# Optimization experiments

Hardware: AMD Instinct MI355X
Metric: run time of the kernel (lower is better)

The kernel has to match this reference:

```python
import jax, jax.numpy as jnp
import numpy as np

B, N, E, H = 4, 2048, 512, 8
D = E // H  # head dim = 64


def setup_inputs() -> dict:
    key = jax.random.key(0)
    ks = jax.random.split(key, 5)
    s = 1.0 / np.sqrt(E)
    return {
        "x": jax.random.normal(ks[0], (B, N, E), dtype=jnp.float32),
        "Wk": jax.random.normal(ks[1], (E, E), dtype=jnp.float32) * s,
        "bk": jax.random.normal(ks[2], (E,), dtype=jnp.float32) * s,
        "Wv": jax.random.normal(ks[3], (E, E), dtype=jnp.float32) * s,
        "bv": jax.random.normal(ks[4], (E,), dtype=jnp.float32) * s,
    }


def reference(x, Wk, bk, Wv, bv):
    b, n, e = x.shape
    # Linear projections (torch Linear: y = x @ W.T + b), split into heads.
    keys = (x @ Wk.T + bk).reshape(b, n, H, D).transpose(0, 2, 1, 3)    # b h n d
    values = (x @ Wv.T + bv).reshape(b, n, H, D).transpose(0, 2, 1, 3)  # b h n d
    # Q = K self-attention: scores [b, h, n, n]
    dotprod = jnp.einsum('bhnd,bhmd->bhnm', keys, keys)
    # softmax over last axis, then unusual POST-softmax scaling by sqrt(emb)
    att = jax.nn.softmax(dotprod, axis=-1) / jnp.sqrt(jnp.asarray(e, x.dtype))
    # dropout p=0 -> identity
    out = jnp.einsum('bhnm,bhmd->bhnd', att, values)
    return out.transpose(0, 2, 1, 3).reshape(b, n, e)
```

## Files before the change

### kernel.cpp

```cpp
#include <hip/hip_runtime.h>

typedef __bf16 bf16_t;
typedef bf16_t bf16x8 __attribute__((ext_vector_type(8)));
typedef float f32x4 __attribute__((ext_vector_type(4)));

#define NSEQ 2048
#define EMB 512
#define HEADS 8
#define HD 64
#define BATCH 4
#define LOG2E 1.4426950408889634f

#define MFMA16(a, b, c) __builtin_amdgcn_mfma_f32_16x16x32_bf16(a, b, c, 0, 0, 0)

__global__ __launch_bounds__(256, 2) void proj_kernel(
    const float* __restrict__ x,
    const float* __restrict__ Wk, const float* __restrict__ bk,
    const float* __restrict__ Wv, const float* __restrict__ bv,
    bf16_t* __restrict__ Kh, bf16_t* __restrict__ Vt)
{
  __shared__ union {
    struct {
      __align__(16) bf16_t A[2][128][40];
      __align__(16) bf16_t B[2][128][40];
    } s;
    __align__(16) bf16_t T[128][136];
  } u;

  const int t    = threadIdx.x;
  const int w    = t >> 6;
  const int lane = t & 63;
  const int quad = lane >> 4;
  const int l15  = lane & 15;
  const int wr   = w >> 1, wc = w & 1;
  const int m0   = blockIdx.x * 128;
  const int n0   = blockIdx.y * 128;
  const int zz   = (blockIdx.y >= 4);
  const float* __restrict__ W = zz ? Wv : Wk;
  const int nW = n0 - zz * 512;

  const int sr = t >> 3;
  const int sj = t & 7;
  const int sb = sj >> 2, sc = (sj & 3) * 8;

  float4 pa[4][2], pb[4][2];
  auto prefetch = [&](int k0) {
#pragma unroll
    for (int i = 0; i < 4; ++i) {
      const float* xa = x + (size_t)(m0 + sr + i * 32) * EMB + k0 + sj * 8;
      const float* wa = W + (size_t)(nW + sr + i * 32) * EMB + k0 + sj * 8;
      pa[i][0] = *(const float4*)xa; pa[i][1] = *(const float4*)(xa + 4);
      pb[i][0] = *(const float4*)wa; pb[i][1] = *(const float4*)(wa + 4);
    }
  };
  auto pack8 = [](float4 a, float4 b) -> bf16x8 {
    bf16x8 v;
    v[0] = (bf16_t)a.x; v[1] = (bf16_t)a.y; v[2] = (bf16_t)a.z; v[3] = (bf16_t)a.w;
    v[4] = (bf16_t)b.x; v[5] = (bf16_t)b.y; v[6] = (bf16_t)b.z; v[7] = (bf16_t)b.w;
    return v;
  };

  f32x4 acc[4][4] = {};
  prefetch(0);

  for (int it = 0; it < 8; ++it) {
    __syncthreads();
#pragma unroll
    for (int i = 0; i < 4; ++i) {
      *(bf16x8*)(&u.s.A[sb][sr + i * 32][sc]) = pack8(pa[i][0], pa[i][1]);
      *(bf16x8*)(&u.s.B[sb][sr + i * 32][sc]) = pack8(pb[i][0], pb[i][1]);
    }
    __syncthreads();
    if (it < 7) prefetch((it + 1) * 64);

    bf16x8 af[4][2], bf[4][2];
#pragma unroll
    for (int mt = 0; mt < 4; ++mt)
#pragma unroll
      for (int kk = 0; kk < 2; ++kk)
        af[mt][kk] = *(const bf16x8*)(&u.s.A[kk][wr * 64 + mt * 16 + l15][quad * 8]);
#pragma unroll
    for (int nt = 0; nt < 4; ++nt)
#pragma unroll
      for (int kk = 0; kk < 2; ++kk)
        bf[nt][kk] = *(const bf16x8*)(&u.s.B[kk][wc * 64 + nt * 16 + l15][quad * 8]);
#pragma unroll
    for (int kk = 0; kk < 2; ++kk)
#pragma unroll
      for (int mt = 0; mt < 4; ++mt)
#pragma unroll
        for (int nt = 0; nt < 4; ++nt)
          acc[mt][nt] = MFMA16(af[mt][kk], bf[nt][kk], acc[mt][nt]);
  }

  __syncthreads();

#pragma unroll
  for (int mt = 0; mt < 4; ++mt) {
#pragma unroll
    for (int nt = 0; nt < 4; ++nt) {
      const int F = wc * 64 + nt * 16 + l15;
      const int c = n0 + F;
      const float bb = zz ? bv[c - 512] : bk[c];
#pragma unroll
      for (int reg = 0; reg < 4; ++reg) {
        const int R = wr * 64 + mt * 16 + quad * 4 + reg;
        const float v = acc[mt][nt][reg] + bb;
        if (!zz) u.T[R][F] = (bf16_t)v;
        else     u.T[F][R] = (bf16_t)v;
      }
    }
  }
  __syncthreads();

#pragma unroll
  for (int i = 0; i < 8; ++i) {
    const int q  = t + i * 256;
    const int R  = q >> 4;
    const int C8 = (q & 15) * 8;
    const bf16x8 v = *(const bf16x8*)(&u.T[R][C8]);
    if (!zz) {
      const int gr = m0 + R, b = gr >> 11, n = gr & (NSEQ - 1);
      const int c = n0 + C8, hh = c >> 6, d = c & 63;
      *(bf16x8*)(Kh + (((size_t)(b * HEADS + hh)) * NSEQ + n) * HD + d) = v;
    } else {
      const int cv = n0 + R - 512, hh = cv >> 6, d = cv & 63;
      const int gr = m0 + C8, b = gr >> 11, n = gr & (NSEQ - 1);
      *(bf16x8*)(Vt + (((size_t)(b * HEADS + hh)) * HD + d) * NSEQ + n) = v;
    }
  }
}

__global__ __launch_bounds__(256, 2) void flash_kernel(
    const bf16_t* __restrict__ Kh, const bf16_t* __restrict__ Vt,
    float* __restrict__ out)
{
  __shared__ union {
    struct {
      __align__(16) bf16_t Kl[2][64][40];
      __align__(16) bf16_t Vl[2][64][40];
      __align__(16) bf16_t Pl[4][64][40];
    } s;
    struct {
      __align__(16) float Cb[2][4096];
      __align__(16) float Lb[2][64][4];
    } c;
  } u;

  const int t    = threadIdx.x;
  const int w    = t >> 6;
  const int lane = t & 63;
  const int quad = lane >> 4;
  const int l15  = lane & 15;
  const int rh   = w & 1;
  const int kh   = w >> 1;

  const int bh = blockIdx.x;
  const int b  = bh >> 3, h = bh & 7;
  const int rowbase = blockIdx.y * 128 + rh * 64;

  const bf16_t* __restrict__ Kb = Kh + (size_t)bh * NSEQ * HD;
  const bf16_t* __restrict__ Vb = Vt + (size_t)bh * HD * NSEQ;

  bf16x8 qf[4][2];
#pragma unroll
  for (int nt = 0; nt < 4; ++nt)
#pragma unroll
    for (int kk = 0; kk < 2; ++kk)
      qf[nt][kk] = *(const bf16x8*)(Kb + (size_t)(rowbase + nt * 16 + l15) * HD +
                                    kk * 32 + quad * 8);

  float mlog[4];
#pragma unroll
  for (int nt = 0; nt < 4; ++nt) {
    float ss = 0.f;
#pragma unroll
    for (int kk = 0; kk < 2; ++kk)
#pragma unroll
      for (int j = 0; j < 8; ++j) {
        const float qv = (float)qf[nt][kk][j];
        ss = fmaf(qv, qv, ss);
      }
    ss += __shfl_xor(ss, 16, 64);
    ss += __shfl_xor(ss, 32, 64);
    mlog[nt] = ss * LOG2E;
  }

  const int sr = t >> 3, sj = t & 7;
  const int sb = sj >> 2, sc = (sj & 3) * 8;

  bf16x8 pk[2], pv[2];
  auto prefetch = [&](int kt) {
    const bf16_t* Kt = Kb + (size_t)kt * 64 * HD;
    pk[0] = *(const bf16x8*)(Kt + (size_t)sr * HD + sj * 8);
    pk[1] = *(const bf16x8*)(Kt + (size_t)(sr + 32) * HD + sj * 8);
    pv[0] = *(const bf16x8*)(Vb + (size_t)sr * NSEQ + kt * 64 + sj * 8);
    pv[1] = *(const bf16x8*)(Vb + (size_t)(sr + 32) * NSEQ + kt * 64 + sj * 8);
  };

  f32x4 acco[4][4] = {};
  float lsum[4] = {0.f, 0.f, 0.f, 0.f};

  prefetch(0);

  for (int kt = 0; kt < NSEQ / 64; ++kt) {
    __syncthreads();
    *(bf16x8*)(&u.s.Kl[sb][sr][sc])      = pk[0];
    *(bf16x8*)(&u.s.Kl[sb][sr + 32][sc]) = pk[1];
    *(bf16x8*)(&u.s.Vl[sb][sr][sc])      = pv[0];
    *(bf16x8*)(&u.s.Vl[sb][sr + 32][sc]) = pv[1];
    __syncthreads();
    if (kt + 1 < NSEQ / 64) prefetch(kt + 1);

    bf16x8 kf[2][2];
#pragma unroll
    for (int jt = 0; jt < 2; ++jt)
#pragma unroll
      for (int kk = 0; kk < 2; ++kk)
        kf[jt][kk] =
            *(const bf16x8*)(&u.s.Kl[kk][kh * 32 + jt * 16 + l15][quad * 8]);

    f32x4 st[2][4] = {};
#pragma unroll
    for (int kk = 0; kk < 2; ++kk)
#pragma unroll
      for (int jt = 0; jt < 2; ++jt)
#pragma unroll
        for (int nt = 0; nt < 4; ++nt)
          st[jt][nt] = MFMA16(kf[jt][kk], qf[nt][kk], st[jt][nt]);

#pragma unroll
    for (int jt = 0; jt < 2; ++jt)
#pragma unroll
      for (int nt = 0; nt < 4; ++nt) {
        union { bf16_t hx[4]; uint2 u2; } pw;
#pragma unroll
        for (int reg = 0; reg < 4; ++reg) {
          const float p =
              __builtin_amdgcn_exp2f(fmaf(st[jt][nt][reg], LOG2E, -mlog[nt]));
          lsum[nt] += p;
          pw.hx[reg] = (bf16_t)p;
        }
        *(uint2*)(&u.s.Pl[w][nt * 16 + l15][jt * 16 + quad * 4]) = pw.u2;
      }

    bf16x8 vf[4];
#pragma unroll
    for (int dt = 0; dt < 4; ++dt)
      vf[dt] = *(const bf16x8*)(&u.s.Vl[kh][dt * 16 + l15][quad * 8]);
#pragma unroll
    for (int rt = 0; rt < 4; ++rt) {
      const bf16x8 pf = *(const bf16x8*)(&u.s.Pl[w][rt * 16 + l15][quad * 8]);
#pragma unroll
      for (int dt = 0; dt < 4; ++dt)
        acco[rt][dt] = MFMA16(pf, vf[dt], acco[rt][dt]);
    }
  }

  __syncthreads();
  if (kh == 1) {
#pragma unroll
    for (int rt = 0; rt < 4; ++rt)
#pragma unroll
      for (int dt = 0; dt < 4; ++dt)
        *(f32x4*)(&u.c.Cb[rh][((rt * 4 + dt) * 64 + lane) * 4]) = acco[rt][dt];
#pragma unroll
    for (int nt = 0; nt < 4; ++nt) u.c.Lb[rh][lane][nt] = lsum[nt];
  }
  __syncthreads();
  if (kh == 0) {
#pragma unroll
    for (int rt = 0; rt < 4; ++rt)
#pragma unroll
      for (int dt = 0; dt < 4; ++dt) {
        const f32x4 o = *(const f32x4*)(&u.c.Cb[rh][((rt * 4 + dt) * 64 + lane) * 4]);
        acco[rt][dt] += o;
      }
#pragma unroll
    for (int nt = 0; nt < 4; ++nt) {
      lsum[nt] += u.c.Lb[rh][lane][nt];
      lsum[nt] += __shfl_xor(lsum[nt], 16, 64);
      lsum[nt] += __shfl_xor(lsum[nt], 32, 64);
    }

    const float SCL = 0.044194173824159216f;
#pragma unroll
    for (int rt = 0; rt < 4; ++rt)
#pragma unroll
      for (int reg = 0; reg < 4; ++reg) {
        const float lr = __shfl(lsum[rt], quad * 4 + reg, 64);
        const float f = SCL / lr;
        const int n = rowbase + rt * 16 + quad * 4 + reg;
#pragma unroll
        for (int dt = 0; dt < 4; ++dt)
          out[((size_t)(b * NSEQ + n)) * EMB + h * HD + dt * 16 + l15] =
              acco[rt][dt][reg] * f;
      }
  }
}

extern "C" void kernel_launch(void* const* d_in, const int* in_sizes, int n_in,
                              void* d_out, int out_size, void* d_ws, size_t ws_size,
                              hipStream_t stream) {
  const float* x  = (const float*)d_in[0];
  const float* Wk = (const float*)d_in[1];
  const float* bk = (const float*)d_in[2];
  const float* Wv = (const float*)d_in[3];
  const float* bv = (const float*)d_in[4];
  float* out = (float*)d_out;

  bf16_t* Kh = (bf16_t*)d_ws;
  bf16_t* Vt = Kh + (size_t)BATCH * HEADS * NSEQ * HD;

  dim3 pg(8192 / 128, 1024 / 128);
  proj_kernel<<<pg, 256, 0, stream>>>(x, Wk, bk, Wv, bv, Kh, Vt);

  dim3 fg(BATCH * HEADS, NSEQ / 128);
  flash_kernel<<<fg, 256, 0, stream>>>(Kh, Vt, out);
}
```

Measured before the change: 133.6 us.

## Give each wave private K/V LDS tiles to remove block-wide barriers

Each wave now loads its own 32-key K slice and matching V slice into a wave-private LDS buffer, so the two __syncthreads per key tile are dropped. Waves sharing a key half (rh=0/1) now both fetch the same K/V data, doubling global/L2 traffic and LDS footprint for K/V. The goal is to stop waves stalling on each other every iteration, relying on intra-wave ordering of LDS writes and reads.

Result: slower. 139.6 us (+4.5%).

```diff
diff --git a/kernel.cpp b/kernel.cpp
--- a/kernel.cpp
+++ b/kernel.cpp
@@ -137,9 +137,9 @@
 {
   __shared__ union {
     struct {
-      __align__(16) bf16_t Kl[2][64][40];
-      __align__(16) bf16_t Vl[2][64][40];
-      __align__(16) bf16_t Pl[4][64][40];
+      __align__(16) bf16_t K[4][2][32][40];
+      __align__(16) bf16_t V[4][64][40];
+      __align__(16) bf16_t P[4][64][40];
     } s;
     struct {
       __align__(16) float Cb[2][4096];
@@ -186,16 +186,22 @@
     mlog[nt] = ss * LOG2E;
   }
 
-  const int sr = t >> 3, sj = t & 7;
-  const int sb = sj >> 2, sc = (sj & 3) * 8;
-
-  bf16x8 pk[2], pv[2];
+  const int skr = lane >> 3;
+  const int skc = lane & 7;
+  const int skk = skc >> 2;
+  const int sk8 = (skc & 3) * 8;
+  const int svd = lane >> 2;
+  const int svc = (lane & 3) * 8;
+
+  bf16x8 pk[4], pv[4];
   auto prefetch = [&](int kt) {
-    const bf16_t* Kt = Kb + (size_t)kt * 64 * HD;
-    pk[0] = *(const bf16x8*)(Kt + (size_t)sr * HD + sj * 8);
-    pk[1] = *(const bf16x8*)(Kt + (size_t)(sr + 32) * HD + sj * 8);
-    pv[0] = *(const bf16x8*)(Vb + (size_t)sr * NSEQ + kt * 64 + sj * 8);
-    pv[1] = *(const bf16x8*)(Vb + (size_t)(sr + 32) * NSEQ + kt * 64 + sj * 8);
+    const bf16_t* Kt = Kb + ((size_t)kt * 64 + kh * 32) * HD;
+    const bf16_t* Vp = Vb + (size_t)kt * 64 + kh * 32;
+#pragma unroll
+    for (int i = 0; i < 4; ++i) {
+      pk[i] = *(const bf16x8*)(Kt + (size_t)(skr + i * 8) * HD + skc * 8);
+      pv[i] = *(const bf16x8*)(Vp + (size_t)(svd + i * 16) * NSEQ + (lane & 3) * 8);
+    }
   };
 
   f32x4 acco[4][4] = {};
@@ -204,12 +210,11 @@
   prefetch(0);
 
   for (int kt = 0; kt < NSEQ / 64; ++kt) {
-    __syncthreads();
-    *(bf16x8*)(&u.s.Kl[sb][sr][sc])      = pk[0];
-    *(bf16x8*)(&u.s.Kl[sb][sr + 32][sc]) = pk[1];
-    *(bf16x8*)(&u.s.Vl[sb][sr][sc])      = pv[0];
-    *(bf16x8*)(&u.s.Vl[sb][sr + 32][sc]) = pv[1];
-    __syncthreads();
+#pragma unroll
+    for (int i = 0; i < 4; ++i) {
+      *(bf16x8*)(&u.s.K[w][skk][skr + i * 8][sk8]) = pk[i];
+      *(bf16x8*)(&u.s.V[w][svd + i * 16][svc])     = pv[i];
+    }
     if (kt + 1 < NSEQ / 64) prefetch(kt + 1);
 
     bf16x8 kf[2][2];
@@ -217,8 +222,7 @@
     for (int jt = 0; jt < 2; ++jt)
 #pragma unroll
       for (int kk = 0; kk < 2; ++kk)
-        kf[jt][kk] =
-            *(const bf16x8*)(&u.s.Kl[kk][kh * 32 + jt * 16 + l15][quad * 8]);
+        kf[jt][kk] = *(const bf16x8*)(&u.s.K[w][kk][jt * 16 + l15][quad * 8]);
 
     f32x4 st[2][4] = {};
 #pragma unroll
@@ -241,16 +245,16 @@
           lsum[nt] += p;
           pw.hx[reg] = (bf16_t)p;
         }
-        *(uint2*)(&u.s.Pl[w][nt * 16 + l15][jt * 16 + quad * 4]) = pw.u2;
+        *(uint2*)(&u.s.P[w][nt * 16 + l15][jt * 16 + quad * 4]) = pw.u2;
       }
 
     bf16x8 vf[4];
 #pragma unroll
     for (int dt = 0; dt < 4; ++dt)
-      vf[dt] = *(const bf16x8*)(&u.s.Vl[kh][dt * 16 + l15][quad * 8]);
+      vf[dt] = *(const bf16x8*)(&u.s.V[w][dt * 16 + l15][quad * 8]);
 #pragma unroll
     for (int rt = 0; rt < 4; ++rt) {
-      const bf16x8 pf = *(const bf16x8*)(&u.s.Pl[w][rt * 16 + l15][quad * 8]);
+      const bf16x8 pf = *(const bf16x8*)(&u.s.P[w][rt * 16 + l15][quad * 8]);
 #pragma unroll
       for (int dt = 0; dt < 4; ++dt)
         acco[rt][dt] = MFMA16(pf, vf[dt], acco[rt][dt]);
```

## Software-pipeline flash loop: overlap PV MFMAs of previous tile with current scores

Applied to the files above, without the earlier changes.

Restructures the flash attention inner loop so the P·V accumulation for tile kt-1 runs after the score/exp phase of tile kt. The P buffer in LDS is double-buffered, and V and P fragments are read into registers before the barrier that overwrites K/V staging. The aim is to give the scheduler independent MFMA work to interleave with the exp and LDS traffic, hiding latency. In exchange it holds more registers (pf and vf live across the barrier) and uses more LDS for P, which could hurt occupancy at launch_bounds(256,2).

After: 140.1 us. 1.05x slower.

```diff
diff --git a/kernel.cpp b/kernel.cpp
--- a/kernel.cpp
+++ b/kernel.cpp
@@ -139,7 +139,7 @@
     struct {
       __align__(16) bf16_t Kl[2][64][40];
       __align__(16) bf16_t Vl[2][64][40];
-      __align__(16) bf16_t Pl[4][64][40];
+      __align__(16) bf16_t Pl[2][4][64][40];
     } s;
     struct {
       __align__(16) float Cb[2][4096];
@@ -197,28 +197,24 @@
     pv[0] = *(const bf16x8*)(Vb + (size_t)sr * NSEQ + kt * 64 + sj * 8);
     pv[1] = *(const bf16x8*)(Vb + (size_t)(sr + 32) * NSEQ + kt * 64 + sj * 8);
   };
-
-  f32x4 acco[4][4] = {};
-  float lsum[4] = {0.f, 0.f, 0.f, 0.f};
-
-  prefetch(0);
-
-  for (int kt = 0; kt < NSEQ / 64; ++kt) {
-    __syncthreads();
+  auto stage_store = [&]() {
     *(bf16x8*)(&u.s.Kl[sb][sr][sc])      = pk[0];
     *(bf16x8*)(&u.s.Kl[sb][sr + 32][sc]) = pk[1];
     *(bf16x8*)(&u.s.Vl[sb][sr][sc])      = pv[0];
     *(bf16x8*)(&u.s.Vl[sb][sr + 32][sc]) = pv[1];
-    __syncthreads();
-    if (kt + 1 < NSEQ / 64) prefetch(kt + 1);
-
+  };
+
+  f32x4 acco[4][4] = {};
+  float lsum[4] = {0.f, 0.f, 0.f, 0.f};
+  bf16x8 vf[4], pf[4];
+
+  auto sphase = [&](int slot) {
     bf16x8 kf[2][2];
 #pragma unroll
     for (int jt = 0; jt < 2; ++jt)
 #pragma unroll
       for (int kk = 0; kk < 2; ++kk)
-        kf[jt][kk] =
-            *(const bf16x8*)(&u.s.Kl[kk][kh * 32 + jt * 16 + l15][quad * 8]);
+        kf[jt][kk] = *(const bf16x8*)(&u.s.Kl[kk][kh * 32 + jt * 16 + l15][quad * 8]);
 
     f32x4 st[2][4] = {};
 #pragma unroll
@@ -241,21 +237,42 @@
           lsum[nt] += p;
           pw.hx[reg] = (bf16_t)p;
         }
-        *(uint2*)(&u.s.Pl[w][nt * 16 + l15][jt * 16 + quad * 4]) = pw.u2;
-      }
-
-    bf16x8 vf[4];
+        *(uint2*)(&u.s.Pl[slot][w][nt * 16 + l15][jt * 16 + quad * 4]) = pw.u2;
+      }
+  };
+  auto read_prev = [&](int slot) {
 #pragma unroll
     for (int dt = 0; dt < 4; ++dt)
       vf[dt] = *(const bf16x8*)(&u.s.Vl[kh][dt * 16 + l15][quad * 8]);
 #pragma unroll
-    for (int rt = 0; rt < 4; ++rt) {
-      const bf16x8 pf = *(const bf16x8*)(&u.s.Pl[w][rt * 16 + l15][quad * 8]);
+    for (int rt = 0; rt < 4; ++rt)
+      pf[rt] = *(const bf16x8*)(&u.s.Pl[slot][w][rt * 16 + l15][quad * 8]);
+  };
+  auto pvphase = [&]() {
+#pragma unroll
+    for (int rt = 0; rt < 4; ++rt)
 #pragma unroll
       for (int dt = 0; dt < 4; ++dt)
-        acco[rt][dt] = MFMA16(pf, vf[dt], acco[rt][dt]);
-    }
-  }
+        acco[rt][dt] = MFMA16(pf[rt], vf[dt], acco[rt][dt]);
+  };
+
+  prefetch(0);
+  stage_store();
+  __syncthreads();
+  prefetch(1);
+  sphase(0);
+
+  for (int kt = 1; kt < NSEQ / 64; ++kt) {
+    read_prev((kt - 1) & 1);
+    __syncthreads();
+    stage_store();
+    __syncthreads();
+    if (kt + 1 < NSEQ / 64) prefetch(kt + 1);
+    sphase(kt & 1);
+    pvphase();
+  }
+  read_prev((NSEQ / 64 - 1) & 1);
+  pvphase();
 
   __syncthreads();
   if (kh == 1) {
```
